# Optimization experiments

Measured on AMD Instinct MI355X. Metric: run time of the kernel, lower is better.

## Reference

```python
import jax, jax.numpy as jnp
import numpy as np

INSIZE = 1024
OUTSIZE = 1024
BATCH = 4096
SIGMA_MIN = 0.1
SIGMA_MAX = 1.0


def setup_inputs() -> dict:
    key = jax.random.key(0)
    k1, k2, k3, k4 = jax.random.split(key, 4)
    x = jax.random.normal(k1, (BATCH, INSIZE), dtype=jnp.float32)
    # torch init: triu(randn); lower part is unused by the math anyway
    U = jnp.triu(jax.random.normal(k2, (INSIZE, INSIZE), dtype=jnp.float32))
    V = jnp.triu(jax.random.normal(k3, (OUTSIZE, OUTSIZE), dtype=jnp.float32))
    p = 0.001 * jax.random.normal(k4, (min(INSIZE, OUTSIZE),), dtype=jnp.float32)
    bias = jnp.zeros((1, OUTSIZE), dtype=jnp.float32)
    return {"x": x, "U": U, "V": V, "p": p, "bias": bias}


def _householder_chain(x, rows):
    # rows: [n_refl, dim]. Row i of the (masked) triu matrix has zeros in its
    # first i entries, which is exactly equivalent to torch Hprod's slicing
    # x[:, -k:] with k = dim - i: the zero prefix leaves x[:, :-k] untouched
    # and the dot/outer-product only involve u[-k:].
    def step(x, u):
        alpha = 2.0 * (x @ u) / jnp.dot(u, u)  # [bs]
        return x - alpha[:, None] * u[None, :], None
    x, _ = jax.lax.scan(step, x, rows)
    return x


def reference(x, U, V, p, bias):
    r = (SIGMA_MAX - SIGMA_MIN) / 2.0
    sigma_mean = SIGMA_MIN + r
    Um = jnp.triu(U)
    Vm = jnpueses = None
    Vm = jnp.triu(V)
    # Umultiply: reflections i = 0 .. insize-1 with k = insize - i
    x = _householder_chain(x, Um)
    # Sigma: insize == outsize -> pure diagonal scaling
    sig = 2.0 * r * (jax.nn.sigmoid(p) - 0.5) + sigma_mean
    x = x * sig[None, :]
    # Vmultiply: reflections i = outsize-1 .. 0 with k = outsize - i
    x = _householder_chain(x, Vm[::-1])
    return x + bias
```

## Files before the change

kernel.cpp:

```cpp
#include <hip/hip_runtime.h>

#define DIM 1024
#define BATCH 4096

typedef __attribute__((ext_vector_type(8))) short short8v;
typedef __attribute__((ext_vector_type(4))) short short4v;
typedef __attribute__((ext_vector_type(4))) float f32x4;

__device__ __forceinline__ float dpp_reduce_bcast(float x) {
  int v = __builtin_bit_cast(int, x);
#define DPP_STEP(ctrl)                                                        \
  {                                                                           \
    int s = __builtin_amdgcn_update_dpp(0, v, ctrl, 0xf, 0xf, true);          \
    v = __builtin_bit_cast(                                                   \
        int, __builtin_bit_cast(float, v) + __builtin_bit_cast(float, s));    \
  }
  DPP_STEP(0x111) DPP_STEP(0x112) DPP_STEP(0x114) DPP_STEP(0x118)
  DPP_STEP(0x142) DPP_STEP(0x143)
#undef DPP_STEP
  return __builtin_bit_cast(float, __builtin_amdgcn_readlane(v, 63));
}

__device__ __forceinline__ short f2bf(float f) {
  unsigned u = __builtin_bit_cast(unsigned, f);
  u += 0x7FFFu + ((u >> 16) & 1u);
  return (short)(u >> 16);
}
__device__ __forceinline__ float bf2f(short h) {
  unsigned u = ((unsigned)(unsigned short)h) << 16;
  return __builtin_bit_cast(float, u);
}

__global__ __launch_bounds__(256) void prep_k(const float* __restrict__ U,
                                              const float* __restrict__ V,
                                              const float* __restrict__ p,
                                              float* __restrict__ tinu,
                                              float* __restrict__ tinv,
                                              float* __restrict__ sg) {
  int gi = blockIdx.x * 256 + threadIdx.x;
  if (gi < DIM) sg[gi] = 0.1f + 0.9f / (1.0f + __expf(-p[gi]));
  int gw = gi >> 6;
  int lane = threadIdx.x & 63;
  if (gw >= 2048) return;
  const float* src = (gw < 1024) ? (U + (size_t)gw * DIM)
                                 : (V + (size_t)(1023 - (gw - 1024)) * DIM);
  float s = 0.f;
#pragma unroll
  for (int q = 0; q < 4; ++q) {
    float4 v = *reinterpret_cast<const float4*>(src + q * 256 + lane * 4);
    s += v.x * v.x + v.y * v.y + v.z * v.z + v.w * v.w;
  }
  float tot = dpp_reduce_bcast(s);
  if (lane == 0) {
    float val = 2.0f / tot;
    if (gw < 1024) tinu[gw] = val; else tinv[gw - 1024] = val;
  }
}

__global__ __launch_bounds__(256) void asplit_k(const float* __restrict__ U,
                                                const float* __restrict__ V,
                                                short* __restrict__ AuH,
                                                short* __restrict__ AuL,
                                                short* __restrict__ AvH,
                                                short* __restrict__ AvL) {
  int e = (blockIdx.x * 256 + threadIdx.x) * 8;
  int side = e >> 20;
  int idx = e & 1048575;
  int r = idx >> 10, c = idx & 1023;
  const float* src = side ? (V + (size_t)(1023 - r) * DIM + c)
                          : (U + (size_t)r * DIM + c);
  float4 a = *reinterpret_cast<const float4*>(src);
  float4 b = *reinterpret_cast<const float4*>(src + 4);
  float fv[8] = {a.x, a.y, a.z, a.w, b.x, b.y, b.z, b.w};
  short8v h, l;
#pragma unroll
  for (int j = 0; j < 8; ++j) {
    short hh = f2bf(fv[j]);
    h[j] = hh;
    l[j] = f2bf(fv[j] - bf2f(hh));
  }
  *reinterpret_cast<short8v*>((side ? AvH : AuH) + idx) = h;
  *reinterpret_cast<short8v*>((side ? AvL : AuL) + idx) = l;
}

__global__ __launch_bounds__(256) void xsplit_k(const float* __restrict__ x,
                                                short* __restrict__ xH,
                                                short* __restrict__ xL) {
  int idx = (blockIdx.x * 256 + threadIdx.x) * 8;
  float4 a = *reinterpret_cast<const float4*>(x + idx);
  float4 b = *reinterpret_cast<const float4*>(x + idx + 4);
  float fv[8] = {a.x, a.y, a.z, a.w, b.x, b.y, b.z, b.w};
  short8v h, l;
#pragma unroll
  for (int j = 0; j < 8; ++j) {
    short hh = f2bf(fv[j]);
    h[j] = hh;
    l[j] = f2bf(fv[j] - bf2f(hh));
  }
  *reinterpret_cast<short8v*>(xH + idx) = h;
  *reinterpret_cast<short8v*>(xL + idx) = l;
}

__global__ __launch_bounds__(256) void tsplUV_k(const float* __restrict__ U,
                                                const float* __restrict__ V,
                                                short* __restrict__ AuTh,
                                                short* __restrict__ AuTl,
                                                short* __restrict__ AvTh,
                                                short* __restrict__ AvTl) {
  __shared__ float tile[64][68];
  const int side = blockIdx.z;
  const int rb = blockIdx.y * 64, cb = blockIdx.x * 64;
  const int f = threadIdx.x;
  const float* S = side ? V : U;
#pragma unroll
  for (int ii = 0; ii < 4; ++ii) {
    int flat = f + ii * 256;
    int r = flat >> 4, c4 = (flat & 15) << 2;
    int rs = rb + r;
    if (side) rs = 1023 - rs;
    float4 v = *reinterpret_cast<const float4*>(S + (size_t)rs * DIM + cb + c4);
    tile[r][c4 + 0] = v.x; tile[r][c4 + 1] = v.y; tile[r][c4 + 2] = v.z; tile[r][c4 + 3] = v.w;
  }
  __syncthreads();
#pragma unroll
  for (int ii = 0; ii < 2; ++ii) {
    int flat = f + ii * 256;
    int cc = flat >> 3, r8 = (flat & 7) << 3;
    short8v vh, vl;
#pragma unroll
    for (int j = 0; j < 8; ++j) {
      float fv = tile[r8 + j][cc];
      short hh = f2bf(fv);
      vh[j] = hh;
      vl[j] = f2bf(fv - bf2f(hh));
    }
    size_t off = (size_t)(cb + cc) * DIM + rb + r8;
    *reinterpret_cast<short8v*>((side ? AvTh : AuTh) + off) = vh;
    *reinterpret_cast<short8v*>((side ? AvTl : AuTl) + off) = vl;
  }
}

__global__ __launch_bounds__(256) void gram_k(const float* __restrict__ U,
                                              const float* __restrict__ V,
                                              const short* __restrict__ AuH,
                                              const short* __restrict__ AuL,
                                              const short* __restrict__ AvH,
                                              const short* __restrict__ AvL,
                                              float* __restrict__ Gu,
                                              float* __restrict__ Gv) {
  __shared__ short Ah[64][36], Al[64][36], Bh[64][36], Bl[64][36];
  const int side = blockIdx.z;
  const float* A = side ? V : U;
  const short* BH = side ? AvH : AuH;
  const short* BL = side ? AvL : AuL;
  float* G = side ? Gv : Gu;
  const int tid = threadIdx.x;
  const int bn = blockIdx.x, bm = blockIdx.y;
  const int wid = tid >> 6, wr = wid >> 1, wc = wid & 1;
  const int lane = tid & 63, l15 = lane & 15, k8 = (lane >> 4) << 3;
  f32x4 acc[2][2] = {};

  for (int kb = 0; kb < DIM; kb += 32) {
    __syncthreads();
#pragma unroll
    for (int ii = 0; ii < 2; ++ii) {
      int flat = tid + ii * 256;
      int r = flat >> 3, kq = (flat & 7) << 2;
      int rg = bm * 64 + r;
      int rs = side ? (1023 - rg) : rg;
      float4 v = *reinterpret_cast<const float4*>(A + (size_t)rs * DIM + kb + kq);
      short4v h, l;
      float fv[4] = {v.x, v.y, v.z, v.w};
#pragma unroll
      for (int j = 0; j < 4; ++j) {
        short hh = f2bf(fv[j]); h[j] = hh; l[j] = f2bf(fv[j] - bf2f(hh));
      }
      *reinterpret_cast<short4v*>(&Ah[r][kq]) = h;
      *reinterpret_cast<short4v*>(&Al[r][kq]) = l;
    }
    {
      int n = tid >> 2, k8s = (tid & 3) << 3;
      size_t off = (size_t)(bn * 64 + n) * DIM + kb + k8s;
      *reinterpret_cast<short8v*>(&Bh[n][k8s]) = *reinterpret_cast<const short8v*>(BH + off);
      *reinterpret_cast<short8v*>(&Bl[n][k8s]) = *reinterpret_cast<const short8v*>(BL + off);
    }
    __syncthreads();
    short8v ah[2], al_[2], bh[2], bl_[2];
#pragma unroll
    for (int m = 0; m < 2; ++m) {
      int r = wr * 32 + m * 16 + l15;
      ah[m] = *reinterpret_cast<const short8v*>(&Ah[r][k8]);
      al_[m] = *reinterpret_cast<const short8v*>(&Al[r][k8]);
    }
#pragma unroll
    for (int n = 0; n < 2; ++n) {
      int r = wc * 32 + n * 16 + l15;
      bh[n] = *reinterpret_cast<const short8v*>(&Bh[r][k8]);
      bl_[n] = *reinterpret_cast<const short8v*>(&Bl[r][k8]);
    }
#pragma unroll
    for (int m = 0; m < 2; ++m)
#pragma unroll
      for (int n = 0; n < 2; ++n) {
        acc[m][n] = __builtin_amdgcn_mfma_f32_16x16x32_bf16(ah[m], bh[n], acc[m][n], 0, 0, 0);
        acc[m][n] = __builtin_amdgcn_mfma_f32_16x16x32_bf16(ah[m], bl_[n], acc[m][n], 0, 0, 0);
        acc[m][n] = __builtin_amdgcn_mfma_f32_16x16x32_bf16(al_[m], bh[n], acc[m][n], 0, 0, 0);
      }
  }
#pragma unroll
  for (int n = 0; n < 2; ++n) {
    int gcol = bn * 64 + wc * 32 + n * 16 + l15;
#pragma unroll
    for (int m = 0; m < 2; ++m) {
      int grow0 = bm * 64 + wr * 32 + m * 16 + ((lane >> 4) << 2);
#pragma unroll
      for (int j = 0; j < 4; ++j)
        G[(size_t)(grow0 + j) * DIM + gcol] = acc[m][n][j];
    }
  }
}

__global__ __launch_bounds__(256) void tdiag64_k(const float* __restrict__ Gu,
                                                 const float* __restrict__ Gv,
                                                 const float* __restrict__ tinu,
                                                 const float* __restrict__ tinv,
                                                 float* __restrict__ Tu,
                                                 float* __restrict__ Tv,
                                                 short* __restrict__ TtuH,
                                                 short* __restrict__ TtuL,
                                                 short* __restrict__ TtvH,
                                                 short* __restrict__ TtvL) {
  __shared__ float B[64][65];
  __shared__ float T[64][65];
  __shared__ float Wb[1024];
  int z = blockIdx.x >> 4;
  int d = blockIdx.x & 15;
  const float* G = z ? Gv : Gu;
  const float* tau = z ? tinv : tinu;
  float* Tg = z ? Tv : Tu;
  short* TH = z ? TtvH : TtuH;
  short* TL = z ? TtvL : TtuL;
  int b0 = d * 64;
  int tid = threadIdx.x;

  for (int e = tid; e < 4096; e += 256) {
    int r = e >> 6, c = e & 63;
    float v;
    if (r < c) v = G[(size_t)(b0 + r) * DIM + b0 + c];
    else if (r == c) v = 1.0f / tau[b0 + r];
    else v = 0.f;
    B[r][c] = v;
    T[r][c] = 0.f;
  }
  __syncthreads();

  if (tid < 16) {
    int o = tid * 4;
    float X[4][4];
#pragma unroll
    for (int k = 0; k < 4; ++k) {
      X[k][k] = 1.0f / B[o + k][o + k];
#pragma unroll
      for (int i = 2; i >= 0; --i) {
        if (i < k) {
          float s = 0.f;
#pragma unroll
          for (int j = 0; j < 4; ++j)
            if (j > i && j <= k) s = fmaf(B[o + i][o + j], X[j][k], s);
          X[i][k] = -s / B[o + i][o + i];
        }
      }
    }
#pragma unroll
    for (int k = 0; k < 4; ++k)
#pragma unroll
      for (int i = 0; i < 4; ++i)
        if (i <= k) T[o + i][o + k] = X[i][k];
  }
  __syncthreads();

  for (int s = 4; s <= 32; s <<= 1) {
    int ss = s * s;
    int tot = (32 / s) * ss;
    for (int e = tid; e < tot; e += 256) {
      int p = e / ss;
      int rem = e - p * ss;
      int m = rem / s;
      int j = rem - m * s;
      int o = p * 2 * s;
      float acc = 0.f;
      for (int l = 0; l < s; ++l)
        acc = fmaf(B[o + m][o + s + l], T[o + s + l][o + s + j], acc);
      Wb[e] = acc;
    }
    __syncthreads();
    for (int e = tid; e < tot; e += 256) {
      int p = e / ss;
      int rem = e - p * ss;
      int i = rem / s;
      int j = rem - i * s;
      int o = p * 2 * s;
      float acc = 0.f;
      for (int m = 0; m < s; ++m)
        acc = fmaf(T[o + i][o + m], Wb[p * ss + m * s + j], acc);
      T[o + i][o + s + j] = -acc;
    }
    __syncthreads();
  }

  for (int e = tid; e < 1024; e += 256) {
    int r = e >> 4, c4 = (e & 15) << 2;
    float4 v;
    v.x = T[r][c4]; v.y = T[r][c4 + 1]; v.z = T[r][c4 + 2]; v.w = T[r][c4 + 3];
    *reinterpret_cast<float4*>(Tg + (size_t)(b0 + r) * DIM + b0 + c4) = v;
  }
  for (int e = tid; e < 512; e += 256) {
    int c = e >> 3, r8 = (e & 7) << 3;
    short8v h, l;
#pragma unroll
    for (int j = 0; j < 8; ++j) {
      float fv = T[r8 + j][c];
      short hh = f2bf(fv);
      h[j] = hh;
      l[j] = f2bf(fv - bf2f(hh));
    }
    size_t off = (size_t)(b0 + c) * DIM + b0 + r8;
    *reinterpret_cast<short8v*>(TH + off) = h;
    *reinterpret_cast<short8v*>(TL + off) = l;
  }
}

__global__ __launch_bounds__(256) void tcomb64_k(const float* __restrict__ Gu,
                                                 const float* __restrict__ Gv,
                                                 float* __restrict__ Tu,
                                                 float* __restrict__ Tv,
                                                 short* __restrict__ TtuH,
                                                 short* __restrict__ TtuL,
                                                 short* __restrict__ TtvH,
                                                 short* __restrict__ TtvL) {
  __shared__ float TA[64][68], SS[64][68], TB[64][68], W[64][68];
  int zz = blockIdx.x;
  int side = zz >> 3, p = zz & 7;
  int a0 = p * 128;
  const float* G = side ? Gv : Gu;
  float* T = side ? Tv : Tu;
  short* TH = side ? TtvH : TtuH;
  short* TL = side ? TtvL : TtuL;
  int tid = threadIdx.x;
#pragma unroll
  for (int ii = 0; ii < 4; ++ii) {
    int flat = tid + ii * 256;
    int r = flat >> 4, c4 = (flat & 15) << 2;
    *reinterpret_cast<float4*>(&TA[r][c4]) =
        *reinterpret_cast<const float4*>(T + (size_t)(a0 + r) * DIM + a0 + c4);
    *reinterpret_cast<float4*>(&SS[r][c4]) =
        *reinterpret_cast<const float4*>(G + (size_t)(a0 + r) * DIM + a0 + 64 + c4);
    *reinterpret_cast<float4*>(&TB[r][c4]) =
        *reinterpret_cast<const float4*>(T + (size_t)(a0 + 64 + r) * DIM + a0 + 64 + c4);
  }
  __syncthreads();
  int tx = tid & 15, ty = tid >> 4;
  float acc[4][4] = {};
  for (int k = 0; k < 64; ++k) {
    float a[4], b[4];
#pragma unroll
    for (int m = 0; m < 4; ++m) a[m] = SS[ty * 4 + m][k];
#pragma unroll
    for (int n = 0; n < 4; ++n) b[n] = TB[k][tx * 4 + n];
#pragma unroll
    for (int m = 0; m < 4; ++m)
#pragma unroll
      for (int n = 0; n < 4; ++n) acc[m][n] = fmaf(a[m], b[n], acc[m][n]);
  }
#pragma unroll
  for (int m = 0; m < 4; ++m)
#pragma unroll
    for (int n = 0; n < 4; ++n) W[ty * 4 + m][tx * 4 + n] = acc[m][n];
  __syncthreads();
  float acc2[4][4] = {};
  for (int k = 0; k < 64; ++k) {
    float a[4], b[4];
#pragma unroll
    for (int m = 0; m < 4; ++m) a[m] = TA[ty * 4 + m][k];
#pragma unroll
    for (int n = 0; n < 4; ++n) b[n] = W[k][tx * 4 + n];
#pragma unroll
    for (int m = 0; m < 4; ++m)
#pragma unroll
      for (int n = 0; n < 4; ++n) acc2[m][n] = fmaf(a[m], b[n], acc2[m][n]);
  }
#pragma unroll
  for (int m = 0; m < 4; ++m)
#pragma unroll
    for (int n = 0; n < 4; ++n)
      T[(size_t)(a0 + ty * 4 + m) * DIM + a0 + 64 + tx * 4 + n] = -acc2[m][n];
#pragma unroll
  for (int n = 0; n < 4; ++n) {
    short4v h, l;
#pragma unroll
    for (int j = 0; j < 4; ++j) {
      float fv = -acc2[j][n];
      short hh = f2bf(fv);
      h[j] = hh;
      l[j] = f2bf(fv - bf2f(hh));
    }
    size_t off = (size_t)(a0 + 64 + tx * 4 + n) * DIM + a0 + ty * 4;
    *reinterpret_cast<short4v*>(TH + off) = h;
    *reinterpret_cast<short4v*>(TL + off) = l;
  }
}

__global__ __launch_bounds__(256) void tcombgg_k(const float* __restrict__ Gu,
                                                 const float* __restrict__ Gv,
                                                 float* __restrict__ Tu,
                                                 float* __restrict__ Tv,
                                                 short* __restrict__ TtuH,
                                                 short* __restrict__ TtuL,
                                                 short* __restrict__ TtvH,
                                                 short* __restrict__ TtvL,
                                                 short* __restrict__ TmpTh,
                                                 short* __restrict__ TmpTl,
                                                 int s, int npair, int stage) {
  __shared__ short Ah[128][44], Al[128][44], Bh[128][44], Bl[128][44];
  const int z = blockIdx.z;
  const int side = z / npair, p = z % npair;
  const int a0 = p * 2 * s;
  const float* Ab;
  const short* BH; const short* BL;
  int ldb;
  if (stage == 1) {
    Ab = (side ? Gv : Gu) + (size_t)a0 * DIM + (a0 + s);
    BH = (side ? TtvH : TtuH) + (size_t)(a0 + s) * DIM + (a0 + s);
    BL = (side ? TtvL : TtuL) + (size_t)(a0 + s) * DIM + (a0 + s);
    ldb = DIM;
  } else {
    Ab = (side ? Tv : Tu) + (size_t)a0 * DIM + a0;
    BH = TmpTh + (size_t)z * s * s;
    BL = TmpTl + (size_t)z * s * s;
    ldb = s;
  }
  const int tid = threadIdx.x;
  const int bn = blockIdx.x, bm = blockIdx.y;
  const int wid = tid >> 6, wr = wid >> 1, wc = wid & 1;
  const int lane = tid & 63, l15 = lane & 15, k8 = (lane >> 4) << 3;
  f32x4 acc[4][4] = {};

  for (int kb = 0; kb < s; kb += 32) {
    __syncthreads();
#pragma unroll
    for (int ii = 0; ii < 4; ++ii) {
      int flat = tid + ii * 256;
      int r = flat >> 3, kq = (flat & 7) << 2;
      float4 v = *reinterpret_cast<const float4*>(Ab + (size_t)(bm * 128 + r) * DIM + kb + kq);
      short4v h, l;
      float fv[4] = {v.x, v.y, v.z, v.w};
#pragma unroll
      for (int j = 0; j < 4; ++j) {
        short hh = f2bf(fv[j]); h[j] = hh; l[j] = f2bf(fv[j] - bf2f(hh));
      }
      *reinterpret_cast<short4v*>(&Ah[r][kq]) = h;
      *reinterpret_cast<short4v*>(&Al[r][kq]) = l;
    }
#pragma unroll
    for (int ii = 0; ii < 2; ++ii) {
      int flat = tid + ii * 256;
      int n = flat >> 2, kk8 = (flat & 3) << 3;
      size_t off = (size_t)(bn * 128 + n) * ldb + kb + kk8;
      *reinterpret_cast<short8v*>(&Bh[n][kk8]) = *reinterpret_cast<const short8v*>(BH + off);
      *reinterpret_cast<short8v*>(&Bl[n][kk8]) = *reinterpret_cast<const short8v*>(BL + off);
    }
    __syncthreads();
    short8v ah[4], al_[4], bh[4], bl_[4];
#pragma unroll
    for (int m = 0; m < 4; ++m) {
      int r = wr * 64 + m * 16 + l15;
      ah[m] = *reinterpret_cast<const short8v*>(&Ah[r][k8]);
      al_[m] = *reinterpret_cast<const short8v*>(&Al[r][k8]);
    }
#pragma unroll
    for (int n = 0; n < 4; ++n) {
      int r = wc * 64 + n * 16 + l15;
      bh[n] = *reinterpret_cast<const short8v*>(&Bh[r][k8]);
      bl_[n] = *reinterpret_cast<const short8v*>(&Bl[r][k8]);
    }
#pragma unroll
    for (int m = 0; m < 4; ++m)
#pragma unroll
      for (int n = 0; n < 4; ++n) {
        acc[m][n] = __builtin_amdgcn_mfma_f32_16x16x32_bf16(ah[m], bh[n], acc[m][n], 0, 0, 0);
        acc[m][n] = __builtin_amdgcn_mfma_f32_16x16x32_bf16(ah[m], bl_[n], acc[m][n], 0, 0, 0);
        acc[m][n] = __builtin_amdgcn_mfma_f32_16x16x32_bf16(al_[m], bh[n], acc[m][n], 0, 0, 0);
      }
  }
  if (stage == 1) {
    size_t base = (size_t)z * s * s;
#pragma unroll
    for (int n = 0; n < 4; ++n) {
      int gcol = bn * 128 + wc * 64 + n * 16 + l15;
#pragma unroll
      for (int m = 0; m < 4; ++m) {
        int gk0 = bm * 128 + wr * 64 + m * 16 + ((lane >> 4) << 2);
        short4v h, l;
#pragma unroll
        for (int j = 0; j < 4; ++j) {
          float fv = acc[m][n][j];
          short hh = f2bf(fv);
          h[j] = hh;
          l[j] = f2bf(fv - bf2f(hh));
        }
        *reinterpret_cast<short4v*>(TmpTh + base + (size_t)gcol * s + gk0) = h;
        *reinterpret_cast<short4v*>(TmpTl + base + (size_t)gcol * s + gk0) = l;
      }
    }
  } else {
    float* T = side ? Tv : Tu;
    float* Cb = T + (size_t)a0 * DIM + (a0 + s);
    short* TH = side ? TtvH : TtuH;
    short* TL = side ? TtvL : TtuL;
#pragma unroll
    for (int n = 0; n < 4; ++n) {
      int gcol = bn * 128 + wc * 64 + n * 16 + l15;
#pragma unroll
      for (int m = 0; m < 4; ++m) {
        int grow0 = bm * 128 + wr * 64 + m * 16 + ((lane >> 4) << 2);
        short4v h, l;
#pragma unroll
        for (int j = 0; j < 4; ++j) {
          float fv = -acc[m][n][j];
          Cb[(size_t)(grow0 + j) * DIM + gcol] = fv;
          short hh = f2bf(fv);
          h[j] = hh;
          l[j] = f2bf(fv - bf2f(hh));
        }
        size_t off = (size_t)(a0 + s + gcol) * DIM + a0 + grow0;
        *reinterpret_cast<short4v*>(TH + off) = h;
        *reinterpret_cast<short4v*>(TL + off) = l;
      }
    }
  }
}

__global__ __launch_bounds__(256) void pgemm_k(const float* __restrict__ Tu,
                                               const float* __restrict__ Tv,
                                               const short* __restrict__ AuTh,
                                               const short* __restrict__ AuTl,
                                               const short* __restrict__ AvTh,
                                               const short* __restrict__ AvTl,
                                               float* __restrict__ Ptu,
                                               float* __restrict__ Ptv) {
  __shared__ short Ah[64][36], Al[64][36], Bh[64][36], Bl[64][36];
  const int side = blockIdx.z;
  const float* A = side ? Tv : Tu;
  const short* BH = side ? AvTh : AuTh;
  const short* BL = side ? AvTl : AuTl;
  float* Out = side ? Ptv : Ptu;
  const int tid = threadIdx.x;
  const int bn = blockIdx.x, bm = blockIdx.y;
  const int wid = tid >> 6, wr = wid >> 1, wc = wid & 1;
  const int lane = tid & 63, l15 = lane & 15, k8 = (lane >> 4) << 3;
  f32x4 acc[2][2] = {};

  for (int kb = 0; kb < DIM; kb += 32) {
    __syncthreads();
#pragma unroll
    for (int ii = 0; ii < 2; ++ii) {
      int flat = tid + ii * 256;
      int r = flat >> 3, kq = (flat & 7) << 2;
      float4 v = *reinterpret_cast<const float4*>(A + (size_t)(bm * 64 + r) * DIM + kb + kq);
      short4v h, l;
      float fv[4] = {v.x, v.y, v.z, v.w};
#pragma unroll
      for (int j = 0; j < 4; ++j) {
        short hh = f2bf(fv[j]); h[j] = hh; l[j] = f2bf(fv[j] - bf2f(hh));
      }
      *reinterpret_cast<short4v*>(&Ah[r][kq]) = h;
      *reinterpret_cast<short4v*>(&Al[r][kq]) = l;
    }
    {
      int n = tid >> 2, k8s = (tid & 3) << 3;
      size_t off = (size_t)(bn * 64 + n) * DIM + kb + k8s;
      *reinterpret_cast<short8v*>(&Bh[n][k8s]) = *reinterpret_cast<const short8v*>(BH + off);
      *reinterpret_cast<short8v*>(&Bl[n][k8s]) = *reinterpret_cast<const short8v*>(BL + off);
    }
    __syncthreads();
    short8v ah[2], al_[2], bh[2], bl_[2];
#pragma unroll
    for (int m = 0; m < 2; ++m) {
      int r = wr * 32 + m * 16 + l15;
      ah[m] = *reinterpret_cast<const short8v*>(&Ah[r][k8]);
      al_[m] = *reinterpret_cast<const short8v*>(&Al[r][k8]);
    }
#pragma unroll
    for (int n = 0; n < 2; ++n) {
      int r = wc * 32 + n * 16 + l15;
      bh[n] = *reinterpret_cast<const short8v*>(&Bh[r][k8]);
      bl_[n] = *reinterpret_cast<const short8v*>(&Bl[r][k8]);
    }
#pragma unroll
    for (int m = 0; m < 2; ++m)
#pragma unroll
      for (int n = 0; n < 2; ++n) {
        acc[m][n] = __builtin_amdgcn_mfma_f32_16x16x32_bf16(ah[m], bh[n], acc[m][n], 0, 0, 0);
        acc[m][n] = __builtin_amdgcn_mfma_f32_16x16x32_bf16(ah[m], bl_[n], acc[m][n], 0, 0, 0);
        acc[m][n] = __builtin_amdgcn_mfma_f32_16x16x32_bf16(al_[m], bh[n], acc[m][n], 0, 0, 0);
      }
  }
#pragma unroll
  for (int n = 0; n < 2; ++n) {
    int gcol = bn * 64 + wc * 32 + n * 16 + l15;
#pragma unroll
    for (int m = 0; m < 2; ++m) {
      int grow0 = bm * 64 + wr * 32 + m * 16 + ((lane >> 4) << 2);
      float4 o;
      o.x = acc[m][n][0]; o.y = acc[m][n][1]; o.z = acc[m][n][2]; o.w = acc[m][n][3];
      *reinterpret_cast<float4*>(Out + (size_t)gcol * DIM + grow0) = o;
    }
  }
}

__global__ __launch_bounds__(256) void ngemm_k(const float* __restrict__ Ptu,
                                               const float* __restrict__ Ptv,
                                               const short* __restrict__ AuTh,
                                               const short* __restrict__ AuTl,
                                               const short* __restrict__ AvTh,
                                               const short* __restrict__ AvTl,
                                               const float* __restrict__ sg,
                                               short* __restrict__ QupH,
                                               short* __restrict__ QupL,
                                               float* __restrict__ Qvt) {
  __shared__ short Ah[64][36], Al[64][36], Bh[64][36], Bl[64][36];
  const int side = blockIdx.z;
  const float* A = side ? Ptv : Ptu;
  const short* BH = side ? AvTh : AuTh;
  const short* BL = side ? AvTl : AuTl;
  const int tid = threadIdx.x;
  const int bn = blockIdx.x, bm = blockIdx.y;
  const int wid = tid >> 6, wr = wid >> 1, wc = wid & 1;
  const int lane = tid & 63, l15 = lane & 15, k8 = (lane >> 4) << 3;
  f32x4 acc[2][2] = {};

  for (int kb = 0; kb < DIM; kb += 32) {
    __syncthreads();
#pragma unroll
    for (int ii = 0; ii < 2; ++ii) {
      int flat = tid + ii * 256;
      int r = flat >> 3, kq = (flat & 7) << 2;
      float4 v = *reinterpret_cast<const float4*>(A + (size_t)(bm * 64 + r) * DIM + kb + kq);
      short4v h, l;
      float fv[4] = {v.x, v.y, v.z, v.w};
#pragma unroll
      for (int j = 0; j < 4; ++j) {
        short hh = f2bf(fv[j]); h[j] = hh; l[j] = f2bf(fv[j] - bf2f(hh));
      }
      *reinterpret_cast<short4v*>(&Ah[r][kq]) = h;
      *reinterpret_cast<short4v*>(&Al[r][kq]) = l;
    }
    {
      int n = tid >> 2, k8s = (tid & 3) << 3;
      size_t off = (size_t)(bn * 64 + n) * DIM + kb + k8s;
      *reinterpret_cast<short8v*>(&Bh[n][k8s]) = *reinterpret_cast<const short8v*>(BH + off);
      *reinterpret_cast<short8v*>(&Bl[n][k8s]) = *reinterpret_cast<const short8v*>(BL + off);
    }
    __syncthreads();
    short8v ah[2], al_[2], bh[2], bl_[2];
#pragma unroll
    for (int m = 0; m < 2; ++m) {
      int r = wr * 32 + m * 16 + l15;
      ah[m] = *reinterpret_cast<const short8v*>(&Ah[r][k8]);
      al_[m] = *reinterpret_cast<const short8v*>(&Al[r][k8]);
    }
#pragma unroll
    for (int n = 0; n < 2; ++n) {
      int r = wc * 32 + n * 16 + l15;
      bh[n] = *reinterpret_cast<const short8v*>(&Bh[r][k8]);
      bl_[n] = *reinterpret_cast<const short8v*>(&Bl[r][k8]);
    }
#pragma unroll
    for (int m = 0; m < 2; ++m)
#pragma unroll
      for (int n = 0; n < 2; ++n) {
        acc[m][n] = __builtin_amdgcn_mfma_f32_16x16x32_bf16(ah[m], bh[n], acc[m][n], 0, 0, 0);
        acc[m][n] = __builtin_amdgcn_mfma_f32_16x16x32_bf16(ah[m], bl_[n], acc[m][n], 0, 0, 0);
        acc[m][n] = __builtin_amdgcn_mfma_f32_16x16x32_bf16(al_[m], bh[n], acc[m][n], 0, 0, 0);
      }
  }
#pragma unroll
  for (int n = 0; n < 2; ++n) {
    int gcol = bn * 64 + wc * 32 + n * 16 + l15;
#pragma unroll
    for (int m = 0; m < 2; ++m) {
      int grow0 = bm * 64 + wr * 32 + m * 16 + ((lane >> 4) << 2);
      if (side == 0) {
        short4v h, l;
#pragma unroll
        for (int j = 0; j < 4; ++j) {
          int row = grow0 + j;
          float del = (row == gcol) ? 1.0f : 0.0f;
          float q = (del - acc[m][n][j]) * sg[row];
          short hh = f2bf(q);
          h[j] = hh;
          l[j] = f2bf(q - bf2f(hh));
        }
        *reinterpret_cast<short4v*>(QupH + (size_t)gcol * DIM + grow0) = h;
        *reinterpret_cast<short4v*>(QupL + (size_t)gcol * DIM + grow0) = l;
      } else {
#pragma unroll
        for (int j = 0; j < 4; ++j) {
          int row = grow0 + j;
          float del = (row == gcol) ? 1.0f : 0.0f;
          Qvt[(size_t)row * DIM + gcol] = del - acc[m][n][j];
        }
      }
    }
  }
}

__global__ __launch_bounds__(256) void mgemm2_k(const float* __restrict__ Qvt,
                                                const short* __restrict__ QupH,
                                                const short* __restrict__ QupL,
                                                short* __restrict__ MTh,
                                                short* __restrict__ MTl) {
  __shared__ short Ah[64][36], Al[64][36], Bh[64][36], Bl[64][36];
  const int tid = threadIdx.x;
  const int bn = blockIdx.x, bm = blockIdx.y;
  const int wid = tid >> 6, wr = wid >> 1, wc = wid & 1;
  const int lane = tid & 63, l15 = lane & 15, k8 = (lane >> 4) << 3;
  f32x4 acc[2][2] = {};

  for (int kb = 0; kb < DIM; kb += 32) {
    __syncthreads();
#pragma unroll
    for (int ii = 0; ii < 2; ++ii) {
      int flat = tid + ii * 256;
      int r = flat >> 3, kq = (flat & 7) << 2;
      float4 v = *reinterpret_cast<const float4*>(Qvt + (size_t)(bm * 64 + r) * DIM + kb + kq);
      short4v h, l;
      float fv[4] = {v.x, v.y, v.z, v.w};
#pragma unroll
      for (int j = 0; j < 4; ++j) {
        short hh = f2bf(fv[j]); h[j] = hh; l[j] = f2bf(fv[j] - bf2f(hh));
      }
      *reinterpret_cast<short4v*>(&Ah[r][kq]) = h;
      *reinterpret_cast<short4v*>(&Al[r][kq]) = l;
    }
    {
      int n = tid >> 2, k8s = (tid & 3) << 3;
      size_t off = (size_t)(bn * 64 + n) * DIM + kb + k8s;
      *reinterpret_cast<short8v*>(&Bh[n][k8s]) = *reinterpret_cast<const short8v*>(QupH + off);
      *reinterpret_cast<short8v*>(&Bl[n][k8s]) = *reinterpret_cast<const short8v*>(QupL + off);
    }
    __syncthreads();
    short8v ah[2], al_[2], bh[2], bl_[2];
#pragma unroll
    for (int m = 0; m < 2; ++m) {
      int r = wr * 32 + m * 16 + l15;
      ah[m] = *reinterpret_cast<const short8v*>(&Ah[r][k8]);
      al_[m] = *reinterpret_cast<const short8v*>(&Al[r][k8]);
    }
#pragma unroll
    for (int n = 0; n < 2; ++n) {
      int r = wc * 32 + n * 16 + l15;
      bh[n] = *reinterpret_cast<const short8v*>(&Bh[r][k8]);
      bl_[n] = *reinterpret_cast<const short8v*>(&Bl[r][k8]);
    }
#pragma unroll
    for (int m = 0; m < 2; ++m)
#pragma unroll
      for (int n = 0; n < 2; ++n) {
        acc[m][n] = __builtin_amdgcn_mfma_f32_16x16x32_bf16(ah[m], bh[n], acc[m][n], 0, 0, 0);
        acc[m][n] = __builtin_amdgcn_mfma_f32_16x16x32_bf16(ah[m], bl_[n], acc[m][n], 0, 0, 0);
        acc[m][n] = __builtin_amdgcn_mfma_f32_16x16x32_bf16(al_[m], bh[n], acc[m][n], 0, 0, 0);
      }
  }
#pragma unroll
  for (int n = 0; n < 2; ++n) {
    int gcol = bn * 64 + wc * 32 + n * 16 + l15;
#pragma unroll
    for (int m = 0; m < 2; ++m) {
      int grow0 = bm * 64 + wr * 32 + m * 16 + ((lane >> 4) << 2);
#pragma unroll
      for (int j = 0; j < 4; ++j) {
        float fv = acc[m][n][j];
        short hh = f2bf(fv);
        MTh[(size_t)(grow0 + j) * DIM + gcol] = hh;
        MTl[(size_t)(grow0 + j) * DIM + gcol] = f2bf(fv - bf2f(hh));
      }
    }
  }
}

__global__ __launch_bounds__(256) void gemm_mfma_k(const short* __restrict__ xH,
                                                   const short* __restrict__ xL,
                                                   const short* __restrict__ Bthi,
                                                   const short* __restrict__ Btlo,
                                                   const float* __restrict__ bias,
                                                   float* __restrict__ out) {
  __shared__ short Ah[128][36], Al[128][36], Bh[64][36], Bl[64][36];
  const int tid = threadIdx.x;
  const int bn = blockIdx.x;
  const int bm = blockIdx.y;
  const int wid = tid >> 6, wr = wid >> 1, wc = wid & 1;
  const int lane = tid & 63, l15 = lane & 15, k8 = (lane >> 4) << 3;
  f32x4 acc[4][2] = {};

  for (int kb = 0; kb < DIM; kb += 32) {
    __syncthreads();
#pragma unroll
    for (int ii = 0; ii < 2; ++ii) {
      int flat = tid + ii * 256;
      int r = flat >> 2, k8s = (flat & 3) << 3;
      size_t off = (size_t)(bm * 128 + r) * DIM + kb + k8s;
      *reinterpret_cast<short8v*>(&Ah[r][k8s]) = *reinterpret_cast<const short8v*>(xH + off);
      *reinterpret_cast<short8v*>(&Al[r][k8s]) = *reinterpret_cast<const short8v*>(xL + off);
    }
    {
      int n = tid >> 2, k8s = (tid & 3) << 3;
      size_t off = (size_t)(bn * 64 + n) * DIM + kb + k8s;
      *reinterpret_cast<short8v*>(&Bh[n][k8s]) = *reinterpret_cast<const short8v*>(Bthi + off);
      *reinterpret_cast<short8v*>(&Bl[n][k8s]) = *reinterpret_cast<const short8v*>(Btlo + off);
    }
    __syncthreads();

    short8v ah[4], al_[4], bh[2], bl_[2];
#pragma unroll
    for (int m = 0; m < 4; ++m) {
      int r = wr * 64 + m * 16 + l15;
      ah[m] = *reinterpret_cast<const short8v*>(&Ah[r][k8]);
      al_[m] = *reinterpret_cast<const short8v*>(&Al[r][k8]);
    }
#pragma unroll
    for (int n = 0; n < 2; ++n) {
      int r = wc * 32 + n * 16 + l15;
      bh[n] = *reinterpret_cast<const short8v*>(&Bh[r][k8]);
      bl_[n] = *reinterpret_cast<const short8v*>(&Bl[r][k8]);
    }
#pragma unroll
    for (int m = 0; m < 4; ++m)
#pragma unroll
      for (int n = 0; n < 2; ++n) {
        acc[m][n] = __builtin_amdgcn_mfma_f32_16x16x32_bf16(ah[m], bh[n], acc[m][n], 0, 0, 0);
        acc[m][n] = __builtin_amdgcn_mfma_f32_16x16x32_bf16(ah[m], bl_[n], acc[m][n], 0, 0, 0);
        acc[m][n] = __builtin_amdgcn_mfma_f32_16x16x32_bf16(al_[m], bh[n], acc[m][n], 0, 0, 0);
      }
  }

#pragma unroll
  for (int n = 0; n < 2; ++n) {
    int gcol = bn * 64 + wc * 32 + n * 16 + l15;
    float bv = bias[gcol];
#pragma unroll
    for (int m = 0; m < 4; ++m) {
      int grow0 = bm * 128 + wr * 64 + m * 16 + ((lane >> 4) << 2);
#pragma unroll
      for (int j = 0; j < 4; ++j)
        out[(size_t)(grow0 + j) * DIM + gcol] = acc[m][n][j] + bv;
    }
  }
}

extern "C" void kernel_launch(void* const* d_in, const int* in_sizes, int n_in,
                              void* d_out, int out_size, void* d_ws, size_t ws_size,
                              hipStream_t stream) {
  const float* x    = (const float*)d_in[0];
  const float* U    = (const float*)d_in[1];
  const float* V    = (const float*)d_in[2];
  const float* p    = (const float*)d_in[3];
  const float* bias = (const float*)d_in[4];
  float* out = (float*)d_out;

  float* F = (float*)d_ws;
  short* AuH  = (short*)F;
  short* AuL  = AuH + 1048576;
  short* AvH  = AuL + 1048576;
  short* AvL  = AvH + 1048576;
  short* QupH = AuH;
  short* QupL = AuL;
  float* Qvt  = F + 1048576;
  float* Gu   = F + 2097152;
  float* Gv   = F + 3145728;
  float* Ptu  = Gu;
  float* Ptv  = Gv;
  short* xH   = (short*)(F + 2097152);
  float* Tu   = F + 4194304;
  float* Tv   = F + 5242880;
  short* MTh  = (short*)Tu;
  short* MTl  = MTh + 1048576;
  short* TtuH = (short*)(F + 6291456);
  short* TtuL = TtuH + 1048576;
  short* TtvH = TtuL + 1048576;
  short* TtvL = TtvH + 1048576;
  short* xL   = (short*)(F + 6291456);
  short* AuTh = (short*)(F + 8388608);
  short* AuTl = AuTh + 1048576;
  short* AvTh = AuTl + 1048576;
  short* AvTl = AvTh + 1048576;
  short* TmpTh = (short*)(F + 10485760);
  short* TmpTl = TmpTh + 524288;
  float* tinu = F + 11010048;
  float* tinv = tinu + DIM;
  float* sg   = tinv + DIM;

  prep_k<<<512, 256, 0, stream>>>(U, V, p, tinu, tinv, sg);
  asplit_k<<<1024, 256, 0, stream>>>(U, V, AuH, AuL, AvH, AvL);
  tsplUV_k<<<dim3(16, 16, 2), 256, 0, stream>>>(U, V, AuTh, AuTl, AvTh, AvTl);
  gram_k<<<dim3(16, 16, 2), 256, 0, stream>>>(U, V, AuH, AuL, AvH, AvL, Gu, Gv);
  hipMemsetAsync(Tu, 0, (size_t)4194304 * sizeof(float), stream);
  tdiag64_k<<<32, 256, 0, stream>>>(Gu, Gv, tinu, tinv, Tu, Tv,
                                    TtuH, TtuL, TtvH, TtvL);
  tcomb64_k<<<16, 256, 0, stream>>>(Gu, Gv, Tu, Tv, TtuH, TtuL, TtvH, TtvL);
  tcombgg_k<<<dim3(1, 1, 8), 256, 0, stream>>>(Gu, Gv, Tu, Tv, TtuH, TtuL, TtvH, TtvL, TmpTh, TmpTl, 128, 4, 1);
  tcombgg_k<<<dim3(1, 1, 8), 256, 0, stream>>>(Gu, Gv, Tu, Tv, TtuH, TtuL, TtvH, TtvL, TmpTh, TmpTl, 128, 4, 2);
  tcombgg_k<<<dim3(2, 2, 4), 256, 0, stream>>>(Gu, Gv, Tu, Tv, TtuH, TtuL, TtvH, TtvL, TmpTh, TmpTl, 256, 2, 1);
  tcombgg_k<<<dim3(2, 2, 4), 256, 0, stream>>>(Gu, Gv, Tu, Tv, TtuH, TtuL, TtvH, TtvL, TmpTh, TmpTl, 256, 2, 2);
  tcombgg_k<<<dim3(4, 4, 2), 256, 0, stream>>>(Gu, Gv, Tu, Tv, TtuH, TtuL, TtvH, TtvL, TmpTh, TmpTl, 512, 1, 1);
  tcombgg_k<<<dim3(4, 4, 2), 256, 0, stream>>>(Gu, Gv, Tu, Tv, TtuH, TtuL, TtvH, TtvL, TmpTh, TmpTl, 512, 1, 2);
  pgemm_k<<<dim3(16, 16, 2), 256, 0, stream>>>(Tu, Tv, AuTh, AuTl, AvTh, AvTl, Ptu, Ptv);
  ngemm_k<<<dim3(16, 16, 2), 256, 0, stream>>>(Ptu, Ptv, AuTh, AuTl, AvTh, AvTl, sg, QupH, QupL, Qvt);
  xsplit_k<<<2048, 256, 0, stream>>>(x, xH, xL);
  mgemm2_k<<<dim3(16, 16), 256, 0, stream>>>(Qvt, QupH, QupL, MTh, MTl);
  gemm_mfma_k<<<dim3(16, 32), 256, 0, stream>>>(xH, xL, MTh, MTl, bias, out);
}
```

Before: 325.7 us.

## Exploit triangular structure in gram/pgemm/ngemm and retile final GEMM

The gram kernel now launches only upper-triangular block pairs and starts its K loop where the triangular factors become nonzero. The pgemm and ngemm kernels clip their K ranges to the nonzero bands of triangular operands, and one side of pgemm skips lower blocks entirely. The final x-by-M GEMM drops from 128-row to 64-row tiles with a swizzled 1D grid, giving more blocks and better L2 locality. This removes wasted MFMA work on zero regions, at the cost of correctness depending on the stated triangular sparsity patterns holding exactly.

Result: no change. 319.6 us (-1.9%).

```diff
diff --git a/kernel.cpp b/kernel.cpp
--- a/kernel.cpp
+++ b/kernel.cpp
@@ -150,17 +150,20 @@
                                               float* __restrict__ Gv) {
   __shared__ short Ah[64][36], Al[64][36], Bh[64][36], Bl[64][36];
   const int side = blockIdx.z;
+  int bm = 0, rem = blockIdx.x;
+  while (rem >= 16 - bm) { rem -= 16 - bm; ++bm; }
+  const int bn = bm + rem;
+  const int kb0 = (side ? (15 - bm) : bn) * 64;
   const float* A = side ? V : U;
   const short* BH = side ? AvH : AuH;
   const short* BL = side ? AvL : AuL;
   float* G = side ? Gv : Gu;
   const int tid = threadIdx.x;
-  const int bn = blockIdx.x, bm = blockIdx.y;
   const int wid = tid >> 6, wr = wid >> 1, wc = wid & 1;
   const int lane = tid & 63, l15 = lane & 15, k8 = (lane >> 4) << 3;
   f32x4 acc[2][2] = {};
 
-  for (int kb = 0; kb < DIM; kb += 32) {
+  for (int kb = kb0; kb < DIM; kb += 32) {
     __syncthreads();
 #pragma unroll
     for (int ii = 0; ii < 2; ++ii) {
@@ -550,17 +553,24 @@
                                                float* __restrict__ Ptv) {
   __shared__ short Ah[64][36], Al[64][36], Bh[64][36], Bl[64][36];
   const int side = blockIdx.z;
+  const int bn = blockIdx.x, bm = blockIdx.y;
+  int kb0, kb1;
+  if (side == 0) {
+    if (bn < bm) return;
+    kb0 = bm * 64; kb1 = (bn + 1) * 64;
+  } else {
+    kb0 = (bm > 15 - bn ? bm : 15 - bn) * 64; kb1 = DIM;
+  }
   const float* A = side ? Tv : Tu;
   const short* BH = side ? AvTh : AuTh;
   const short* BL = side ? AvTl : AuTl;
   float* Out = side ? Ptv : Ptu;
   const int tid = threadIdx.x;
-  const int bn = blockIdx.x, bm = blockIdx.y;
   const int wid = tid >> 6, wr = wid >> 1, wc = wid & 1;
   const int lane = tid & 63, l15 = lane & 15, k8 = (lane >> 4) << 3;
   f32x4 acc[2][2] = {};
 
-  for (int kb = 0; kb < DIM; kb += 32) {
+  for (int kb = kb0; kb < kb1; kb += 32) {
     __syncthreads();
 #pragma unroll
     for (int ii = 0; ii < 2; ++ii) {
@@ -630,16 +640,23 @@
                                                float* __restrict__ Qvt) {
   __shared__ short Ah[64][36], Al[64][36], Bh[64][36], Bl[64][36];
   const int side = blockIdx.z;
+  const int bn = blockIdx.x, bm = blockIdx.y;
+  int kb0, kb1;
+  if (side == 0) {
+    kb0 = 0;
+    kb1 = ((bm < bn ? bm : bn) + 1) * 64;
+  } else {
+    kb0 = (15 - bn) * 64; kb1 = DIM;
+  }
   const float* A = side ? Ptv : Ptu;
   const short* BH = side ? AvTh : AuTh;
   const short* BL = side ? AvTl : AuTl;
   const int tid = threadIdx.x;
-  const int bn = blockIdx.x, bm = blockIdx.y;
   const int wid = tid >> 6, wr = wid >> 1, wc = wid & 1;
   const int lane = tid & 63, l15 = lane & 15, k8 = (lane >> 4) << 3;
   f32x4 acc[2][2] = {};
 
-  for (int kb = 0; kb < DIM; kb += 32) {
+  for (int kb = kb0; kb < kb1; kb += 32) {
     __syncthreads();
 #pragma unroll
     for (int ii = 0; ii < 2; ++ii) {
@@ -795,21 +812,20 @@
                                                    const short* __restrict__ Btlo,
                                                    const float* __restrict__ bias,
                                                    float* __restrict__ out) {
-  __shared__ short Ah[128][36], Al[128][36], Bh[64][36], Bl[64][36];
+  __shared__ short Ah[64][36], Al[64][36], Bh[64][36], Bl[64][36];
   const int tid = threadIdx.x;
-  const int bn = blockIdx.x;
-  const int bm = blockIdx.y;
+  int lin = (blockIdx.x & 7) * 128 + (blockIdx.x >> 3);
+  const int bm = lin >> 4;
+  const int bn = lin & 15;
   const int wid = tid >> 6, wr = wid >> 1, wc = wid & 1;
   const int lane = tid & 63, l15 = lane & 15, k8 = (lane >> 4) << 3;
-  f32x4 acc[4][2] = {};
+  f32x4 acc[2][2] = {};
 
   for (int kb = 0; kb < DIM; kb += 32) {
     __syncthreads();
-#pragma unroll
-    for (int ii = 0; ii < 2; ++ii) {
-      int flat = tid + ii * 256;
-      int r = flat >> 2, k8s = (flat & 3) << 3;
-      size_t off = (size_t)(bm * 128 + r) * DIM + kb + k8s;
+    {
+      int r = tid >> 2, k8s = (tid & 3) << 3;
+      size_t off = (size_t)(bm * 64 + r) * DIM + kb + k8s;
       *reinterpret_cast<short8v*>(&Ah[r][k8s]) = *reinterpret_cast<const short8v*>(xH + off);
       *reinterpret_cast<short8v*>(&Al[r][k8s]) = *reinterpret_cast<const short8v*>(xL + off);
     }
@@ -821,10 +837,10 @@
     }
     __syncthreads();
 
-    short8v ah[4], al_[4], bh[2], bl_[2];
-#pragma unroll
-    for (int m = 0; m < 4; ++m) {
-      int r = wr * 64 + m * 16 + l15;
+    short8v ah[2], al_[2], bh[2], bl_[2];
+#pragma unroll
+    for (int m = 0; m < 2; ++m) {
+      int r = wr * 32 + m * 16 + l15;
       ah[m] = *reinterpret_cast<const short8v*>(&Ah[r][k8]);
       al_[m] = *reinterpret_cast<const short8v*>(&Al[r][k8]);
     }
@@ -835,7 +851,7 @@
       bl_[n] = *reinterpret_cast<const short8v*>(&Bl[r][k8]);
     }
 #pragma unroll
-    for (int m = 0; m < 4; ++m)
+    for (int m = 0; m < 2; ++m)
 #pragma unroll
       for (int n = 0; n < 2; ++n) {
         acc[m][n] = __builtin_amdgcn_mfma_f32_16x16x32_bf16(ah[m], bh[n], acc[m][n], 0, 0, 0);
@@ -849,8 +865,8 @@
     int gcol = bn * 64 + wc * 32 + n * 16 + l15;
     float bv = bias[gcol];
 #pragma unroll
-    for (int m = 0; m < 4; ++m) {
-      int grow0 = bm * 128 + wr * 64 + m * 16 + ((lane >> 4) << 2);
+    for (int m = 0; m < 2; ++m) {
+      int grow0 = bm * 64 + wr * 32 + m * 16 + ((lane >> 4) << 2);
 #pragma unroll
       for (int j = 0; j < 4; ++j)
         out[(size_t)(grow0 + j) * DIM + gcol] = acc[m][n][j] + bv;
@@ -903,7 +919,7 @@
   prep_k<<<512, 256, 0, stream>>>(U, V, p, tinu, tinv, sg);
   asplit_k<<<1024, 256, 0, stream>>>(U, V, AuH, AuL, AvH, AvL);
   tsplUV_k<<<dim3(16, 16, 2), 256, 0, stream>>>(U, V, AuTh, AuTl, AvTh, AvTl);
-  gram_k<<<dim3(16, 16, 2), 256, 0, stream>>>(U, V, AuH, AuL, AvH, AvL, Gu, Gv);
+  gram_k<<<dim3(136, 1, 2), 256, 0, stream>>>(U, V, AuH, AuL, AvH, AvL, Gu, Gv);
   hipMemsetAsync(Tu, 0, (size_t)4194304 * sizeof(float), stream);
   tdiag64_k<<<32, 256, 0, stream>>>(Gu, Gv, tinu, tinv, Tu, Tv,
                                     TtuH, TtuL, TtvH, TtvL);
@@ -918,5 +934,5 @@
   ngemm_k<<<dim3(16, 16, 2), 256, 0, stream>>>(Ptu, Ptv, AuTh, AuTl, AvTh, AvTl, sg, QupH, QupL, Qvt);
   xsplit_k<<<2048, 256, 0, stream>>>(x, xH, xL);
   mgemm2_k<<<dim3(16, 16), 256, 0, stream>>>(Qvt, QupH, QupL, MTh, MTl);
-  gemm_mfma_k<<<dim3(16, 32), 256, 0, stream>>>(xH, xL, MTh, MTl, bias, out);
-}
+  gemm_mfma_k<<<1024, 256, 0, stream>>>(xH, xL, MTh, MTl, bias, out);
+}
```
